# Optimization experiments

Hardware: AMD Instinct MI355X
Metric: run time of the kernel (lower is better)

Reference implementation:

```python
import math
import jax, jax.numpy as jnp
import numpy as np

NUM_HEADS = 8
HIDDEN = 512
HEAD_DIM = HIDDEN // NUM_HEADS
LEFT_CONTEXT = 128
RIGHT_CONTEXT = 0


def setup_inputs() -> dict:
    key = jax.random.key(0)
    k1, k2, k3 = jax.random.split(key, 3)
    queries = jax.random.normal(k1, (4, 64, 128, NUM_HEADS, HEAD_DIM), dtype=jnp.float32)
    keys = jax.random.normal(k2, (4, 64, 256, NUM_HEADS, HEAD_DIM), dtype=jnp.float32)
    # pos_proj weight, torch Linear layout [out_features, in_features]
    W_pos = jax.random.normal(k3, (NUM_HEADS * HEAD_DIM, HIDDEN), dtype=jnp.float32) * (1.0 / math.sqrt(HIDDEN))
    return {"queries": queries, "keys": keys, "W_pos": W_pos}


def reference(queries, keys, W_pos):
    batch, num_blocks, block_size, num_heads, head_dim = queries.shape
    context = keys.shape[2]
    left = max(0, LEFT_CONTEXT - 1)
    right = RIGHT_CONTEXT

    # q: [b, h, n, s, d]; k: [b, h, n, d, c]
    q = jnp.transpose(queries, (0, 3, 1, 2, 4))
    k = jnp.transpose(keys, (0, 3, 1, 4, 2))
    term_ac = jnp.matmul(q, k)  # [b, h, n, s, c]

    # sinusoidal relative-position embeddings for offsets left .. -right
    positions = jnp.arange(left, -right - 1, -1, dtype=jnp.float32)  # [P]
    num_timescales = HIDDEN // 2
    log_increment = math.log(10000.0) / max(num_timescales - 1, 1)
    inv_timescales = jnp.exp(jnp.arange(num_timescales, dtype=jnp.float32) * -log_increment)
    scaled_time = positions[:, None] * inv_timescales[None, :]  # [P, HIDDEN/2]
    sin_emb = jnp.concatenate([jnp.sin(scaled_time), jnp.cos(scaled_time)], axis=-1)  # [P, HIDDEN]

    # pos_proj (no bias): [P, H*D] -> [P, H, D]
    proj = (sin_emb @ W_pos.T).reshape(-1, num_heads, head_dim)
    pos_length = proj.shape[0]

    # term_bd: [b, h, n, s, P]
    term_bd = jnp.einsum('bhnsd,phd->bhnsp', q, proj)

    # Transformer-XL relative shift: pad, flatten, truncate, reshape
    pad = context + 1 - pos_length
    if pad > 0:
        term_bd = jnp.pad(term_bd, ((0, 0), (0, 0), (0, 0), (0, 0), (0, pad)))
    term_bd = term_bd.reshape(batch, num_heads, num_blocks, block_size * (context + 1))
    term_bd = term_bd[:, :, :, : block_size * context]
    term_bd = term_bd.reshape(batch, num_heads, num_blocks, block_size, context)

    return term_ac + term_bd
```

## Files before the change

### kernel.cpp

```cpp
#include <hip/hip_runtime.h>
#include <hip/hip_bf16.h>


typedef __bf16 bf16x8 __attribute__((ext_vector_type(8)));
typedef unsigned short u16x8 __attribute__((ext_vector_type(8)));
typedef unsigned int u32x4 __attribute__((ext_vector_type(4)));
typedef float f32x4 __attribute__((ext_vector_type(4)));

__device__ __forceinline__ unsigned short f2bf(float f) {
    unsigned u = __float_as_uint(f);
    u = (u + 0x7FFFu + ((u >> 16) & 1u)) >> 16;
    return (unsigned short)u;
}
__device__ __forceinline__ float bf2f(unsigned short s) {
    return __uint_as_float(((unsigned)s) << 16);
}
__device__ __forceinline__ unsigned pk2(float a, float b) {
    return (__float_as_uint(a) >> 16) | (__float_as_uint(b) & 0xFFFF0000u);
}

__device__ __forceinline__ void barrier_no_vm_drain() {
    asm volatile("s_waitcnt lgkmcnt(0)" ::: "memory");
    __builtin_amdgcn_s_barrier();
}

__global__ __launch_bounds__(256) void proj_kernel(const float* __restrict__ W,
                                                   unsigned short* __restrict__ projw) {
    __shared__ float se[512];
    int bid = blockIdx.x;
    int p  = bid >> 3;
    int jq = bid & 7;
    int t = threadIdx.x;
    const float LOGINC = (float)(9.210340371976184 / 255.0);
    float pos = (float)(127 - p);
    float inv = expf(-LOGINC * (float)t);
    float ang = pos * inv;
    se[t]       = sinf(ang);
    se[t + 256] = cosf(ang);
    __syncthreads();
    int j  = jq * 64 + (t >> 2);
    int tq = t & 3;
    const float4* wr = (const float4*)(W + (size_t)j * 512 + tq * 128);
    const float4* sr = (const float4*)(se + tq * 128);
    float a = 0.f;
#pragma unroll
    for (int i = 0; i < 32; ++i) {
        float4 wv = wr[i];
        float4 sv = sr[i];
        a += sv.x * wv.x + sv.y * wv.y + sv.z * wv.z + sv.w * wv.w;
    }
    a += __shfl_xor(a, 1);
    a += __shfl_xor(a, 2);
    if (tq == 0) projw[p * 512 + j] = f2bf(a);
}

__global__ __launch_bounds__(256, 4) void fused_kernel(const float* __restrict__ Q,
                                                       const float* __restrict__ Kg,
                                                       const unsigned short* __restrict__ projw,
                                                       float* __restrict__ out) {
    __shared__ unsigned short BDs[128 * 128];
    __shared__ unsigned short Klds[2][32 * 64];

    int bid = blockIdx.x;
    int wid = (bid & 7) * 256 + (bid >> 3);
    int h = wid & 7;
    int n = (wid >> 3) & 63;
    int b = wid >> 9;

    const float* qbase = Q  + ((size_t)(b * 64 + n) * 128) * 512 + h * 64;
    const float* kbase = Kg + ((size_t)(b * 64 + n) * 256) * 512 + h * 64;

    int tid = threadIdx.x;
    int w  = tid >> 6;
    int l  = tid & 63;
    int lo = l & 15;
    int hi = l >> 4;
    int rq = l >> 4;
    int cq = l & 15;

    float4 qv[4];
    {
        const float* ar = qbase + (size_t)(w * 32 + 0 * 16 + lo) * 512;
        qv[0] = *(const float4*)(ar + 0 * 32 + hi * 8);
        qv[1] = *(const float4*)(ar + 0 * 32 + hi * 8 + 4);
        qv[2] = *(const float4*)(ar + 1 * 32 + hi * 8);
        qv[3] = *(const float4*)(ar + 1 * 32 + hi * 8 + 4);
    }
    float4 qv2[4];
    {
        const float* ar = qbase + (size_t)(w * 32 + 1 * 16 + lo) * 512;
        qv2[0] = *(const float4*)(ar + 0 * 32 + hi * 8);
        qv2[1] = *(const float4*)(ar + 0 * 32 + hi * 8 + 4);
        qv2[2] = *(const float4*)(ar + 1 * 32 + hi * 8);
        qv2[3] = *(const float4*)(ar + 1 * 32 + hi * 8 + 4);
    }

    float4 kpre[2][2];
#pragma unroll
    for (int it = 0; it < 2; ++it) {
        int row = w * 8 + it * 4 + rq;
        kpre[0][it] = *(const float4*)(kbase + (size_t)(0 * 32 + row) * 512 + cq * 4);
    }
#pragma unroll
    for (int it = 0; it < 2; ++it) {
        int row = w * 8 + it * 4 + rq;
        kpre[1][it] = *(const float4*)(kbase + (size_t)(1 * 32 + row) * 512 + cq * 4);
    }

    bf16x8 afrag[2][2];
#pragma unroll
    for (int kk = 0; kk < 2; ++kk) {
        float4 va = qv[kk * 2], vb = qv[kk * 2 + 1];
        u16x8 u;
        u[0] = f2bf(va.x); u[1] = f2bf(va.y); u[2] = f2bf(va.z); u[3] = f2bf(va.w);
        u[4] = f2bf(vb.x); u[5] = f2bf(vb.y); u[6] = f2bf(vb.z); u[7] = f2bf(vb.w);
        afrag[0][kk] = __builtin_bit_cast(bf16x8, u);
    }
#pragma unroll
    for (int kk = 0; kk < 2; ++kk) {
        float4 va = qv2[kk * 2], vb = qv2[kk * 2 + 1];
        u16x8 u;
        u[0] = f2bf(va.x); u[1] = f2bf(va.y); u[2] = f2bf(va.z); u[3] = f2bf(va.w);
        u[4] = f2bf(vb.x); u[5] = f2bf(vb.y); u[6] = f2bf(vb.z); u[7] = f2bf(vb.w);
        afrag[1][kk] = __builtin_bit_cast(bf16x8, u);
    }

    const unsigned short* pbase = projw + h * 64;
#pragma unroll 2
    for (int pj = 0; pj < 8; ++pj) {
        int prow = pj * 16 + lo;
        const unsigned short* pr = pbase + (size_t)prow * 512;
        bf16x8 pf0 = *(const bf16x8*)(pr + hi * 8);
        bf16x8 pf1 = *(const bf16x8*)(pr + 32 + hi * 8);
#pragma unroll
        for (int i2 = 0; i2 < 2; ++i2) {
            f32x4 acc = {0.f, 0.f, 0.f, 0.f};
            acc = __builtin_amdgcn_mfma_f32_16x16x32_bf16(pf0, afrag[i2][0], acc, 0, 0, 0);
            acc = __builtin_amdgcn_mfma_f32_16x16x32_bf16(pf1, afrag[i2][1], acc, 0, 0, 0);
            int s  = w * 32 + i2 * 16 + lo;
            int pb = pj * 16 + hi * 4;
#pragma unroll
            for (int jr = 0; jr < 4; ++jr) {
                int cw = (s + pb + jr) & 127;
                BDs[s * 128 + (cw ^ ((s & 7) << 3))] = f2bf(acc[jr]);
            }
        }
    }

    size_t obase = ((size_t)((b * 8 + h) * 64 + n)) * (128 * 256);

#pragma unroll
    for (int ch = 0; ch < 8; ++ch) {
        const int buf = ch & 1;
#pragma unroll
        for (int it = 0; it < 2; ++it) {
            int row = w * 8 + it * 4 + rq;
            float4 v = kpre[buf][it];
            uint2 pk;
            pk.x = pk2(v.x, v.y);
            pk.y = pk2(v.z, v.w);
            *reinterpret_cast<uint2*>(&Klds[buf][row * 64 + ((cq * 4) ^ ((row & 7) << 3))]) = pk;
        }
        if (ch < 6) {
#pragma unroll
            for (int it = 0; it < 2; ++it) {
                int row = w * 8 + it * 4 + rq;
                kpre[buf][it] =
                    *(const float4*)(kbase + (size_t)((ch + 2) * 32 + row) * 512 + cq * 4);
            }
        }
        barrier_no_vm_drain();

#pragma unroll
        for (int cjl = 0; cjl < 2; ++cjl) {
            int cj  = ch * 2 + cjl;
            int krl = cjl * 16 + lo;
            bf16x8 kf0 = *(const bf16x8*)&Klds[buf][krl * 64 + ((hi * 8)      ^ ((krl & 7) << 3))];
            bf16x8 kf1 = *(const bf16x8*)&Klds[buf][krl * 64 + ((32 + hi * 8) ^ ((krl & 7) << 3))];
#pragma unroll
            for (int i2 = 0; i2 < 2; ++i2) {
                int stile = 2 * w + i2;
                f32x4 acc = {0.f, 0.f, 0.f, 0.f};
                acc = __builtin_amdgcn_mfma_f32_16x16x32_bf16(kf0, afrag[i2][0], acc, 0, 0, 0);
                acc = __builtin_amdgcn_mfma_f32_16x16x32_bf16(kf1, afrag[i2][1], acc, 0, 0, 0);
                int s  = stile * 16 + lo;
                int cb = cj * 16 + hi * 4;
                if (cj >= stile && cj <= stile + 8) {
                    uint2 pk = *(const uint2*)&BDs[s * 128 + ((cb & 127) ^ ((s & 7) << 3))];
                    unsigned short v0 = (unsigned short)(pk.x & 0xffffu);
                    unsigned short v1 = (unsigned short)(pk.x >> 16);
                    unsigned short v2 = (unsigned short)(pk.y & 0xffffu);
                    unsigned short v3 = (unsigned short)(pk.y >> 16);
                    if ((unsigned)(cb + 0 - s) < 128u) acc[0] += bf2f(v0);
                    if ((unsigned)(cb + 1 - s) < 128u) acc[1] += bf2f(v1);
                    if ((unsigned)(cb + 2 - s) < 128u) acc[2] += bf2f(v2);
                    if ((unsigned)(cb + 3 - s) < 128u) acc[3] += bf2f(v3);
                }
                *reinterpret_cast<float4*>(&out[obase + (size_t)s * 256 + cb]) =
                    *reinterpret_cast<float4*>(&acc);
            }
        }
    }
}

extern "C" void kernel_launch(void* const* d_in, const int* in_sizes, int n_in,
                              void* d_out, int out_size, void* d_ws, size_t ws_size,
                              hipStream_t stream) {
    const float* Q  = (const float*)d_in[0];
    const float* Kg = (const float*)d_in[1];
    const float* W  = (const float*)d_in[2];
    float* out = (float*)d_out;
    unsigned short* projw = (unsigned short*)d_ws;

    hipLaunchKernelGGL(proj_kernel, dim3(1024), dim3(256), 0, stream, W, projw);
    hipLaunchKernelGGL(fused_kernel, dim3(2048), dim3(256), 0, stream, Q, Kg, projw, out);
}
```

Baseline: 136.9 us.

## Split each query block across two workgroups to halve LDS and raise occupancy

Each workgroup now handles 64 query rows of a (b,h,n) block instead of 128, so the grid doubles to 4096 and each wave processes one 16-row tile. The BD scratch in LDS shrinks by half, and launch bounds rise from 4 to 6 blocks per CU to allow more resident waves. The cost is that every K tile is loaded and converted twice, once per half-block, which doubles K global traffic and the K-side conversion work.

Measured after the change: 145.1 us. 6.0% more time.

```diff
diff --git a/kernel.cpp b/kernel.cpp
--- a/kernel.cpp
+++ b/kernel.cpp
@@ -54,20 +54,21 @@
     if (tq == 0) projw[p * 512 + j] = f2bf(a);
 }
 
-__global__ __launch_bounds__(256, 4) void fused_kernel(const float* __restrict__ Q,
+__global__ __launch_bounds__(256, 6) void fused_kernel(const float* __restrict__ Q,
                                                        const float* __restrict__ Kg,
                                                        const unsigned short* __restrict__ projw,
                                                        float* __restrict__ out) {
-    __shared__ unsigned short BDs[128 * 128];
+    __shared__ unsigned short BDs[64 * 128];
     __shared__ unsigned short Klds[2][32 * 64];
 
     int bid = blockIdx.x;
-    int wid = (bid & 7) * 256 + (bid >> 3);
-    int h = wid & 7;
-    int n = (wid >> 3) & 63;
-    int b = wid >> 9;
+    int wid = (bid & 7) * 512 + (bid >> 3);
+    int sub = wid & 1;
+    int h = (wid >> 1) & 7;
+    int n = (wid >> 4) & 63;
+    int b = wid >> 10;
 
-    const float* qbase = Q  + ((size_t)(b * 64 + n) * 128) * 512 + h * 64;
+    const float* qbase = Q  + ((size_t)((b * 64 + n) * 128 + sub * 64)) * 512 + h * 64;
     const float* kbase = Kg + ((size_t)(b * 64 + n) * 256) * 512 + h * 64;
 
     int tid = threadIdx.x;
@@ -78,21 +79,16 @@
     int rq = l >> 4;
     int cq = l & 15;
 
+    int s_loc = w * 16 + lo;
+    int s_g   = sub * 64 + s_loc;
+
     float4 qv[4];
     {
-        const float* ar = qbase + (size_t)(w * 32 + 0 * 16 + lo) * 512;
-        qv[0] = *(const float4*)(ar + 0 * 32 + hi * 8);
-        qv[1] = *(const float4*)(ar + 0 * 32 + hi * 8 + 4);
-        qv[2] = *(const float4*)(ar + 1 * 32 + hi * 8);
-        qv[3] = *(const float4*)(ar + 1 * 32 + hi * 8 + 4);
-    }
-    float4 qv2[4];
-    {
-        const float* ar = qbase + (size_t)(w * 32 + 1 * 16 + lo) * 512;
-        qv2[0] = *(const float4*)(ar + 0 * 32 + hi * 8);
-        qv2[1] = *(const float4*)(ar + 0 * 32 + hi * 8 + 4);
-        qv2[2] = *(const float4*)(ar + 1 * 32 + hi * 8);
-        qv2[3] = *(const float4*)(ar + 1 * 32 + hi * 8 + 4);
+        const float* ar = qbase + (size_t)s_loc * 512;
+        qv[0] = *(const float4*)(ar + hi * 8);
+        qv[1] = *(const float4*)(ar + hi * 8 + 4);
+        qv[2] = *(const float4*)(ar + 32 + hi * 8);
+        qv[3] = *(const float4*)(ar + 32 + hi * 8 + 4);
     }
 
     float4 kpre[2][2];
@@ -107,22 +103,14 @@
         kpre[1][it] = *(const float4*)(kbase + (size_t)(1 * 32 + row) * 512 + cq * 4);
     }
 
-    bf16x8 afrag[2][2];
+    bf16x8 afrag[2];
 #pragma unroll
     for (int kk = 0; kk < 2; ++kk) {
         float4 va = qv[kk * 2], vb = qv[kk * 2 + 1];
         u16x8 u;
         u[0] = f2bf(va.x); u[1] = f2bf(va.y); u[2] = f2bf(va.z); u[3] = f2bf(va.w);
         u[4] = f2bf(vb.x); u[5] = f2bf(vb.y); u[6] = f2bf(vb.z); u[7] = f2bf(vb.w);
-        afrag[0][kk] = __builtin_bit_cast(bf16x8, u);
-    }
-#pragma unroll
-    for (int kk = 0; kk < 2; ++kk) {
-        float4 va = qv2[kk * 2], vb = qv2[kk * 2 + 1];
-        u16x8 u;
-        u[0] = f2bf(va.x); u[1] = f2bf(va.y); u[2] = f2bf(va.z); u[3] = f2bf(va.w);
-        u[4] = f2bf(vb.x); u[5] = f2bf(vb.y); u[6] = f2bf(vb.z); u[7] = f2bf(vb.w);
-        afrag[1][kk] = __builtin_bit_cast(bf16x8, u);
+        afrag[kk] = __builtin_bit_cast(bf16x8, u);
     }
 
     const unsigned short* pbase = projw + h * 64;
@@ -132,22 +120,19 @@
         const unsigned short* pr = pbase + (size_t)prow * 512;
         bf16x8 pf0 = *(const bf16x8*)(pr + hi * 8);
         bf16x8 pf1 = *(const bf16x8*)(pr + 32 + hi * 8);
+        f32x4 acc = {0.f, 0.f, 0.f, 0.f};
+        acc = __builtin_amdgcn_mfma_f32_16x16x32_bf16(pf0, afrag[0], acc, 0, 0, 0);
+        acc = __builtin_amdgcn_mfma_f32_16x16x32_bf16(pf1, afrag[1], acc, 0, 0, 0);
+        int pb = pj * 16 + hi * 4;
 #pragma unroll
-        for (int i2 = 0; i2 < 2; ++i2) {
-            f32x4 acc = {0.f, 0.f, 0.f, 0.f};
-            acc = __builtin_amdgcn_mfma_f32_16x16x32_bf16(pf0, afrag[i2][0], acc, 0, 0, 0);
-            acc = __builtin_amdgcn_mfma_f32_16x16x32_bf16(pf1, afrag[i2][1], acc, 0, 0, 0);
-            int s  = w * 32 + i2 * 16 + lo;
-            int pb = pj * 16 + hi * 4;
-#pragma unroll
-            for (int jr = 0; jr < 4; ++jr) {
-                int cw = (s + pb + jr) & 127;
-                BDs[s * 128 + (cw ^ ((s & 7) << 3))] = f2bf(acc[jr]);
-            }
+        for (int jr = 0; jr < 4; ++jr) {
+            int cw = (s_g + pb + jr) & 127;
+            BDs[s_loc * 128 + (cw ^ ((s_loc & 7) << 3))] = f2bf(acc[jr]);
         }
     }
 
-    size_t obase = ((size_t)((b * 8 + h) * 64 + n)) * (128 * 256);
+    size_t obase = ((size_t)((b * 8 + h) * 64 + n)) * (128 * 256) + (size_t)sub * 64 * 256;
+    int stile_g = sub * 4 + w;
 
 #pragma unroll
     for (int ch = 0; ch < 8; ++ch) {
@@ -177,28 +162,23 @@
             int krl = cjl * 16 + lo;
             bf16x8 kf0 = *(const bf16x8*)&Klds[buf][krl * 64 + ((hi * 8)      ^ ((krl & 7) << 3))];
             bf16x8 kf1 = *(const bf16x8*)&Klds[buf][krl * 64 + ((32 + hi * 8) ^ ((krl & 7) << 3))];
-#pragma unroll
-            for (int i2 = 0; i2 < 2; ++i2) {
-                int stile = 2 * w + i2;
-                f32x4 acc = {0.f, 0.f, 0.f, 0.f};
-                acc = __builtin_amdgcn_mfma_f32_16x16x32_bf16(kf0, afrag[i2][0], acc, 0, 0, 0);
-                acc = __builtin_amdgcn_mfma_f32_16x16x32_bf16(kf1, afrag[i2][1], acc, 0, 0, 0);
-                int s  = stile * 16 + lo;
-                int cb = cj * 16 + hi * 4;
-                if (cj >= stile && cj <= stile + 8) {
-                    uint2 pk = *(const uint2*)&BDs[s * 128 + ((cb & 127) ^ ((s & 7) << 3))];
-                    unsigned short v0 = (unsigned short)(pk.x & 0xffffu);
-                    unsigned short v1 = (unsigned short)(pk.x >> 16);
-                    unsigned short v2 = (unsigned short)(pk.y & 0xffffu);
-                    unsigned short v3 = (unsigned short)(pk.y >> 16);
-                    if ((unsigned)(cb + 0 - s) < 128u) acc[0] += bf2f(v0);
-                    if ((unsigned)(cb + 1 - s) < 128u) acc[1] += bf2f(v1);
-                    if ((unsigned)(cb + 2 - s) < 128u) acc[2] += bf2f(v2);
-                    if ((unsigned)(cb + 3 - s) < 128u) acc[3] += bf2f(v3);
-                }
-                *reinterpret_cast<float4*>(&out[obase + (size_t)s * 256 + cb]) =
-                    *reinterpret_cast<float4*>(&acc);
+            f32x4 acc = {0.f, 0.f, 0.f, 0.f};
+            acc = __builtin_amdgcn_mfma_f32_16x16x32_bf16(kf0, afrag[0], acc, 0, 0, 0);
+            acc = __builtin_amdgcn_mfma_f32_16x16x32_bf16(kf1, afrag[1], acc, 0, 0, 0);
+            int cb = cj * 16 + hi * 4;
+            if (cj >= stile_g && cj <= stile_g + 8) {
+                uint2 pk = *(const uint2*)&BDs[s_loc * 128 + ((cb & 127) ^ ((s_loc & 7) << 3))];
+                unsigned short v0 = (unsigned short)(pk.x & 0xffffu);
+                unsigned short v1 = (unsigned short)(pk.x >> 16);
+                unsigned short v2 = (unsigned short)(pk.y & 0xffffu);
+                unsigned short v3 = (unsigned short)(pk.y >> 16);
+                if ((unsigned)(cb + 0 - s_g) < 128u) acc[0] += bf2f(v0);
+                if ((unsigned)(cb + 1 - s_g) < 128u) acc[1] += bf2f(v1);
+                if ((unsigned)(cb + 2 - s_g) < 128u) acc[2] += bf2f(v2);
+                if ((unsigned)(cb + 3 - s_g) < 128u) acc[3] += bf2f(v3);
             }
+            *reinterpret_cast<float4*>(&out[obase + (size_t)s_loc * 256 + cb]) =
+                *reinterpret_cast<float4*>(&acc);
         }
     }
 }
@@ -213,5 +193,5 @@
     unsigned short* projw = (unsigned short*)d_ws;
 
     hipLaunchKernelGGL(proj_kernel, dim3(1024), dim3(256), 0, stream, W, projw);
-    hipLaunchKernelGGL(fused_kernel, dim3(2048), dim3(256), 0, stream, Q, Kg, projw, out);
+    hipLaunchKernelGGL(fused_kernel, dim3(4096), dim3(256), 0, stream, Q, Kg, projw, out);
 }
```
